# Optimization experiments

Measured on AMD Instinct MI355X. Metric: run time of the kernel, lower is better.

## Reference

```python
import jax, jax.numpy as jnp
import numpy as np


def setup_inputs() -> dict:
    key = jax.random.key(0)
    k1, k2, k3 = jax.random.split(key, 3)
    N, K, D = 50000, 32, 128
    x = jax.random.normal(k1, (N, D), dtype=jnp.float32)
    weights = jax.random.uniform(k2, (N, K), dtype=jnp.float32)
    neighbors = jax.random.randint(k3, (N, K), 0, N, dtype=jnp.int64)
    return {"x": x, "weights": weights, "neighbors": neighbors}


def reference(x, weights, neighbors):
    # Per-node importance pooling: normalize weights to sum to 1
    # (uniform fallback when the weight sum is zero), then compute the
    # weighted sum of gathered neighbor features.
    K = weights.shape[1]
    s = jnp.sum(weights, axis=-1, keepdims=True)            # [N, 1]
    safe = jnp.where(s == 0, jnp.float32(1.0), s)
    wn = jnp.where(s == 0, jnp.float32(1.0 / K), weights / safe)  # [N, K]
    feats = x[neighbors]                                    # [N, K, D] gather
    return jnp.einsum('nkd,nk->nd', feats, wn)              # [N, D]
```

## Files before the change

kernel.cpp:

```cpp
#include <hip/hip_runtime.h>
#include <hip/hip_fp16.h>


typedef __attribute__((ext_vector_type(2))) float f32x2;

__global__ __launch_bounds__(256) void quant_rows_u8(
    const float* __restrict__ x,
    unsigned short* __restrict__ xq,
    float* __restrict__ scale,
    int N)
{
    const int lane = threadIdx.x & 63;
    const int row  = blockIdx.x * 4 + (threadIdx.x >> 6);
    if (row >= N) return;

    const f32x2 v = *reinterpret_cast<const f32x2*>(
        x + (size_t)row * 128 + lane * 2);
    float m = fmaxf(fabsf(v.x), fabsf(v.y));
    #pragma unroll
    for (int off = 32; off >= 1; off >>= 1)
        m = fmaxf(m, __shfl_xor(m, off, 64));

    const float inv = (m > 0.0f) ? 127.0f / m : 0.0f;
    const int q0 = (int)rintf(v.x * inv) + 128;
    const int q1 = (int)rintf(v.y * inv) + 128;
    const unsigned int u =
        ((unsigned int)(q1 & 0xFF) << 8) | (unsigned int)(q0 & 0xFF);
    xq[(size_t)row * 64 + lane] = (unsigned short)u;
    if (lane == 0) scale[row] = m * (1.0f / 127.0f);
}

__global__ __launch_bounds__(256) void pack_wn_idx(
    const float* __restrict__ w,
    const int* __restrict__ nbr,
    const float* __restrict__ scale,
    unsigned int* __restrict__ packed,
    int N)
{
    const int lane = threadIdx.x & 63;
    const int k    = lane & 31;
    const int node = blockIdx.x * 8 + ((threadIdx.x >> 6) << 1) + (lane >> 5);
    if (node >= N) return;

    const float wv = w[(size_t)node * 32 + k];
    float s = wv;
    #pragma unroll
    for (int off = 16; off >= 1; off >>= 1)
        s += __shfl_xor(s, off, 64);

    const int   idx  = nbr[(size_t)node * 32 + k];
    const bool  zero = (s == 0.0f);
    const float wn   = zero ? (1.0f / 32.0f) : (wv / s);
    const float ws   = wn * scale[idx];
    const unsigned short h = __half_as_ushort(__float2half(ws));
    packed[(size_t)node * 32 + k] =
        ((unsigned int)h << 16) | (unsigned int)(idx & 0xFFFF);
}

__global__ __launch_bounds__(256) void gather_u8_pair(
    const unsigned int* __restrict__ xq,
    const unsigned int* __restrict__ packed,
    float* __restrict__ out,
    int N)
{
    __shared__ unsigned int pk_lds[256];

    const int t = threadIdx.x;
    {
        const size_t g = (size_t)blockIdx.x * 256 + t;
        pk_lds[t] = (g < (size_t)N * 32) ? packed[g] : 0u;
    }
    __syncthreads();

    const int node_local = t >> 5;
    const int c          = t & 31;
    const int node       = blockIdx.x * 8 + node_local;
    if (node >= N) return;

    const unsigned int* prow = pk_lds + node_local * 32;
    const unsigned int* xc   = xq + c;

    float a0 = 0.0f, a1 = 0.0f, a2 = 0.0f, a3 = 0.0f, sw = 0.0f;
    #pragma unroll
    for (int k = 0; k < 32; ++k) {
        const unsigned int pk  = prow[k];
        const unsigned int idx = pk & 0xFFFFu;
        const float        ws  = __half2float(
            __ushort_as_half((unsigned short)(pk >> 16)));
        const unsigned int u   = xc[(size_t)idx * 32];
        a0 = fmaf(ws, (float)(u & 0xFFu),         a0);
        a1 = fmaf(ws, (float)((u >> 8) & 0xFFu),  a1);
        a2 = fmaf(ws, (float)((u >> 16) & 0xFFu), a2);
        a3 = fmaf(ws, (float)(u >> 24),           a3);
        sw += ws;
    }

    const float b = 128.0f * sw;
    float4 r;
    r.x = a0 - b;
    r.y = a1 - b;
    r.z = a2 - b;
    r.w = a3 - b;
    *reinterpret_cast<float4*>(out + (size_t)node * 128 + c * 4) = r;
}

struct alignas(8) Half4 { __half2 a, b; };

__global__ __launch_bounds__(256) void convert_f32_to_f16(
    const float* __restrict__ x, Half4* __restrict__ xh, int n4)
{
    const int stride = gridDim.x * blockDim.x;
    for (int i = blockIdx.x * blockDim.x + threadIdx.x; i < n4; i += stride) {
        float4 v = reinterpret_cast<const float4*>(x)[i];
        Half4 h;
        h.a = __floats2half2_rn(v.x, v.y);
        h.b = __floats2half2_rn(v.z, v.w);
        xh[i] = h;
    }
}

__global__ __launch_bounds__(256) void importance_pool_f16_cols(
    const __half* __restrict__ xh,
    const float* __restrict__ w,
    const int* __restrict__ nbr,
    float* __restrict__ out,
    int N, int colBase)
{
    constexpr int K = 32;
    constexpr int D = 128;

    const int lane = threadIdx.x & 63;
    int node = blockIdx.x * 4 + (threadIdx.x >> 6);
    if (node >= N) return;
    node = __builtin_amdgcn_readfirstlane(node);

    const float* wrow = w   + (size_t)node * K;
    const int*   nrow = nbr + (size_t)node * K;

    float wk[K];
    float s = 0.0f;
    #pragma unroll
    for (int k = 0; k < K; ++k) { wk[k] = wrow[k]; s += wk[k]; }
    int idx[K];
    #pragma unroll
    for (int k = 0; k < K; ++k) idx[k] = nrow[k];

    const bool  zero = (s == 0.0f);
    const float inv  = zero ? 0.0f : (1.0f / s);
    const float uni  = 1.0f / (float)K;

    const __half* xl = xh + colBase + lane;
    float acc = 0.0f;
    #pragma unroll
    for (int k = 0; k < K; ++k) {
        const float v  = __half2float(xl[(size_t)idx[k] * D]);
        const float wn = zero ? uni : wk[k] * inv;
        acc = fmaf(wn, v, acc);
    }
    out[(size_t)node * D + colBase + lane] = acc;
}

__global__ __launch_bounds__(256) void importance_pool_f32(
    const float* __restrict__ x,
    const float* __restrict__ w,
    const int* __restrict__ nbr,
    float* __restrict__ out,
    int N)
{
    constexpr int K = 32;
    constexpr int D = 128;

    const int lane = threadIdx.x & 63;
    int node = blockIdx.x * 4 + (threadIdx.x >> 6);
    if (node >= N) return;
    node = __builtin_amdgcn_readfirstlane(node);

    const float* wrow = w   + (size_t)node * K;
    const int*   nrow = nbr + (size_t)node * K;

    float wk[K];
    float s = 0.0f;
    #pragma unroll
    for (int k = 0; k < K; ++k) { wk[k] = wrow[k]; s += wk[k]; }

    const bool  zero = (s == 0.0f);
    const float inv  = zero ? 0.0f : (1.0f / s);
    const float uni  = 1.0f / (float)K;

    const int col = lane * 2;
    float ax = 0.0f, ay = 0.0f;
    #pragma unroll
    for (int k = 0; k < K; ++k) {
        const float wn  = zero ? uni : wk[k] * inv;
        const int   idx = nrow[k];
        const float2 v = *reinterpret_cast<const float2*>(
            x + (size_t)idx * D + col);
        ax = fmaf(wn, v.x, ax);
        ay = fmaf(wn, v.y, ay);
    }

    f32x2 r; r.x = ax; r.y = ay;
    *reinterpret_cast<f32x2*>(out + (size_t)node * D + col) = r;
}

extern "C" void kernel_launch(void* const* d_in, const int* in_sizes, int n_in,
                              void* d_out, int out_size, void* d_ws, size_t ws_size,
                              hipStream_t stream) {
    const float* x   = (const float*)d_in[0];
    const float* w   = (const float*)d_in[1];
    const int*   nbr = (const int*)d_in[2];
    float*       out = (float*)d_out;

    const int K = 32;
    const int N = in_sizes[1] / K;
    const int xn = in_sizes[0];

    const size_t xqB      = (size_t)N * 128;
    const size_t packedB  = (size_t)N * K * 4;
    const size_t scaleB   = (size_t)N * 4;
    const size_t needInt8 = xqB + packedB + scaleB;
    const size_t needF16  = (size_t)xn * sizeof(__half);

    if (N <= 65535 && ws_size >= needInt8) {
        unsigned short* xq     = (unsigned short*)d_ws;
        unsigned int*   packed = (unsigned int*)((char*)d_ws + xqB);
        float*          scale  = (float*)((char*)d_ws + xqB + packedB);

        quant_rows_u8<<<(N + 3) / 4, 256, 0, stream>>>(x, xq, scale, N);
        pack_wn_idx<<<(N + 7) / 8, 256, 0, stream>>>(w, nbr, scale, packed, N);
        gather_u8_pair<<<(N + 7) / 8, 256, 0, stream>>>(
            (const unsigned int*)xq, packed, out, N);
    } else if (ws_size >= needF16) {
        const int nodes_per_block = 4;
        const int blocks = (N + nodes_per_block - 1) / nodes_per_block;
        const int n4 = xn / 4;
        convert_f32_to_f16<<<2048, 256, 0, stream>>>(x, (Half4*)d_ws, n4);
        importance_pool_f16_cols<<<blocks, 256, 0, stream>>>(
            (const __half*)d_ws, w, nbr, out, N, 0);
        importance_pool_f16_cols<<<blocks, 256, 0, stream>>>(
            (const __half*)d_ws, w, nbr, out, N, 64);
    } else {
        const int nodes_per_block = 4;
        const int blocks = (N + nodes_per_block - 1) / nodes_per_block;
        importance_pool_f32<<<blocks, 256, 0, stream>>>(x, w, nbr, out, N);
    }
}
```

Measured before the change: 45.70 us.

## Partition neighbors by index half and gather in two cache-friendly passes

The pack kernel now uses a wave ballot to reorder each node's 32 packed neighbor entries so that indices in the lower half of the node range come first, and records per-node counts. The gather is split into two launches: each pass reads only the half of the quantized feature table it needs, and the second pass adds its result into the output. The aim is to shrink the gather's working set so it stays resident in the per-XCD L2. In exchange the branchless loops still issue 32 loads per pass (inactive slots reload a clamped entry), the output is read and written again, and there is one more kernel launch.

```diff
diff --git a/kernel.cpp b/kernel.cpp
--- a/kernel.cpp
+++ b/kernel.cpp
@@ -30,11 +30,12 @@
     if (lane == 0) scale[row] = m * (1.0f / 127.0f);
 }
 
-__global__ __launch_bounds__(256) void pack_wn_idx(
+__global__ __launch_bounds__(256) void pack_partition_u8(
     const float* __restrict__ w,
     const int* __restrict__ nbr,
     const float* __restrict__ scale,
     unsigned int* __restrict__ packed,
+    unsigned char* __restrict__ cnt,
     int N)
 {
     const int lane = threadIdx.x & 63;
@@ -53,55 +54,100 @@
     const float wn   = zero ? (1.0f / 32.0f) : (wv / s);
     const float ws   = wn * scale[idx];
     const unsigned short h = __half_as_ushort(__float2half(ws));
-    packed[(size_t)node * 32 + k] =
+    const unsigned int word =
         ((unsigned int)h << 16) | (unsigned int)(idx & 0xFFFF);
-}
-
-__global__ __launch_bounds__(256) void gather_u8_pair(
+
+    const int CH = (N + 1) >> 1;
+    const bool bit = (idx < CH);
+    const unsigned long long bal = __ballot(bit);
+    const unsigned int gm    = (unsigned int)(bal >> ((lane >> 5) * 32));
+    const unsigned int below = gm & ((1u << k) - 1);
+    const int cnt0 = __popc(gm);
+    const int pos  = bit ? __popc(below) : cnt0 + (k - __popc(below));
+
+    packed[(size_t)node * 32 + pos] = word;
+    if (k == 0) cnt[node] = (unsigned char)cnt0;
+}
+
+__global__ __launch_bounds__(256) void gather_u8_chunk(
     const unsigned int* __restrict__ xq,
     const unsigned int* __restrict__ packed,
+    const unsigned char* __restrict__ cnt,
     float* __restrict__ out,
-    int N)
+    int N, int pass)
 {
     __shared__ unsigned int pk_lds[256];
+    __shared__ int cnt_s[8];
 
     const int t = threadIdx.x;
     {
         const size_t g = (size_t)blockIdx.x * 256 + t;
         pk_lds[t] = (g < (size_t)N * 32) ? packed[g] : 0u;
     }
+    if (t < 8) {
+        const int n8 = blockIdx.x * 8 + t;
+        cnt_s[t] = (n8 < N) ? (int)cnt[n8] : 0;
+    }
     __syncthreads();
 
     const int node_local = t >> 5;
     const int c          = t & 31;
     const int node       = blockIdx.x * 8 + node_local;
-    if (node >= N) return;
-
+
+    const int myc = cnt_s[node_local];
     const unsigned int* prow = pk_lds + node_local * 32;
     const unsigned int* xc   = xq + c;
 
     float a0 = 0.0f, a1 = 0.0f, a2 = 0.0f, a3 = 0.0f, sw = 0.0f;
-    #pragma unroll
-    for (int k = 0; k < 32; ++k) {
-        const unsigned int pk  = prow[k];
-        const unsigned int idx = pk & 0xFFFFu;
-        const float        ws  = __half2float(
-            __ushort_as_half((unsigned short)(pk >> 16)));
-        const unsigned int u   = xc[(size_t)idx * 32];
-        a0 = fmaf(ws, (float)(u & 0xFFu),         a0);
-        a1 = fmaf(ws, (float)((u >> 8) & 0xFFu),  a1);
-        a2 = fmaf(ws, (float)((u >> 16) & 0xFFu), a2);
-        a3 = fmaf(ws, (float)(u >> 24),           a3);
-        sw += ws;
-    }
-
+
+    if (pass == 0) {
+        #pragma unroll
+        for (int k = 0; k < 32; ++k) {
+            const bool act  = (k < myc);
+            const int  slot = act ? k : 0;
+            const unsigned int pk  = prow[slot];
+            const unsigned int idx = pk & 0xFFFFu;
+            float ws = __half2float(
+                __ushort_as_half((unsigned short)(pk >> 16)));
+            ws = act ? ws : 0.0f;
+            const unsigned int u = xc[(size_t)idx * 32];
+            a0 = fmaf(ws, (float)(u & 0xFFu),         a0);
+            a1 = fmaf(ws, (float)((u >> 8) & 0xFFu),  a1);
+            a2 = fmaf(ws, (float)((u >> 16) & 0xFFu), a2);
+            a3 = fmaf(ws, (float)(u >> 24),           a3);
+            sw += ws;
+        }
+    } else {
+        #pragma unroll
+        for (int k = 0; k < 32; ++k) {
+            const bool act  = (k >= myc);
+            const int  slot = act ? k : 31;
+            const unsigned int pk  = prow[slot];
+            const unsigned int idx = pk & 0xFFFFu;
+            float ws = __half2float(
+                __ushort_as_half((unsigned short)(pk >> 16)));
+            ws = act ? ws : 0.0f;
+            const unsigned int u = xc[(size_t)idx * 32];
+            a0 = fmaf(ws, (float)(u & 0xFFu),         a0);
+            a1 = fmaf(ws, (float)((u >> 8) & 0xFFu),  a1);
+            a2 = fmaf(ws, (float)((u >> 16) & 0xFFu), a2);
+            a3 = fmaf(ws, (float)(u >> 24),           a3);
+            sw += ws;
+        }
+    }
+
+    if (node >= N) return;
     const float b = 128.0f * sw;
+    float* po = out + (size_t)node * 128 + c * 4;
     float4 r;
-    r.x = a0 - b;
-    r.y = a1 - b;
-    r.z = a2 - b;
-    r.w = a3 - b;
-    *reinterpret_cast<float4*>(out + (size_t)node * 128 + c * 4) = r;
+    if (pass == 0) {
+        r.x = a0 - b; r.y = a1 - b; r.z = a2 - b; r.w = a3 - b;
+    } else {
+        const float4 p = *reinterpret_cast<const float4*>(po);
+        r.x = p.x + a0 - b; r.y = p.y + a1 - b;
+        r.z = p.z + a2 - b; r.w = p.w + a3 - b;
+    }
+    *reinterpret_cast<float4*>(po) = r;
 }
 
 struct alignas(8) Half4 { __half2 a, b; };
@@ -218,21 +264,25 @@
     const size_t xqB      = (size_t)N * 128;
     const size_t packedB  = (size_t)N * K * 4;
     const size_t scaleB   = (size_t)N * 4;
-    const size_t needInt8 = xqB + packedB + scaleB;
+    const size_t cntB     = (size_t)N;
+    const size_t needInt8 = xqB + packedB + scaleB + cntB;
     const size_t needF16  = (size_t)xn * sizeof(__half);
 
     if (N <= 65535 && ws_size >= needInt8) {
         unsigned short* xq     = (unsigned short*)d_ws;
         unsigned int*   packed = (unsigned int*)((char*)d_ws + xqB);
         float*          scale  = (float*)((char*)d_ws + xqB + packedB);
+        unsigned char*  cnt    = (unsigned char*)((char*)d_ws + xqB + packedB + scaleB);
 
         quant_rows_u8<<<(N + 3) / 4, 256, 0, stream>>>(x, xq, scale, N);
-        pack_wn_idx<<<(N + 7) / 8, 256, 0, stream>>>(w, nbr, scale, packed, N);
-        gather_u8_pair<<<(N + 7) / 8, 256, 0, stream>>>(
-            (const unsigned int*)xq, packed, out, N);
+        pack_partition_u8<<<(N + 7) / 8, 256, 0, stream>>>(
+            w, nbr, scale, packed, cnt, N);
+        gather_u8_chunk<<<(N + 7) / 8, 256, 0, stream>>>(
+            (const unsigned int*)xq, packed, cnt, out, N, 0);
+        gather_u8_chunk<<<(N + 7) / 8, 256, 0, stream>>>(
+            (const unsigned int*)xq, packed, cnt, out, N, 1);
     } else if (ws_size >= needF16) {
-        const int nodes_per_block = 4;
-        const int blocks = (N + nodes_per_block - 1) / nodes_per_block;
+        const int blocks = (N + 3) / 4;
         const int n4 = xn / 4;
         convert_f32_to_f16<<<2048, 256, 0, stream>>>(x, (Half4*)d_ws, n4);
         importance_pool_f16_cols<<<blocks, 256, 0, stream>>>(
@@ -240,8 +290,7 @@
         importance_pool_f16_cols<<<blocks, 256, 0, stream>>>(
             (const __half*)d_ws, w, nbr, out, N, 64);
     } else {
-        const int nodes_per_block = 4;
-        const int blocks = (N + nodes_per_block - 1) / nodes_per_block;
+        const int blocks = (N + 3) / 4;
         importance_pool_f32<<<blocks, 256, 0, stream>>>(x, w, nbr, out, N);
     }
 }
```

New measurement: 70.96 us. +55.3%, slower.
